# Kernel tuning notes

Measured on AMD Instinct MI355X. Metric: run time of the kernel, lower is better.

Reference implementation:

```python
import jax, jax.numpy as jnp
import numpy as np

N_USER = 100_000
N_WALLET = 100_000
E = 1_600_000
HID, OUT = 128, 64
H, C = 4, 32  # GAT heads, per-head channels (HID // 4)
U_IN, W_IN = 16, 4
EPS = 1e-5


def _sage(x_src, x_dst, ei, w_l, b_l, w_r):
    """PyG SAGEConv (mean aggr): lin_l(mean_j x_j) + lin_r(x_i)."""
    src, dst = ei[0], ei[1]
    n = x_dst.shape[0]
    s = jax.ops.segment_sum(x_src[src], dst, num_segments=n)
    deg = jax.ops.segment_sum(jnp.ones((src.shape[0],), x_src.dtype), dst, num_segments=n)
    agg = s / jnp.maximum(deg, 1.0)[:, None]
    return agg @ w_l + b_l + x_dst @ w_r


def _bn(x, g, b):
    """BatchNorm over node dim (training-mode batch stats)."""
    m = x.mean(0)
    v = x.var(0)
    return (x - m) * jax.lax.rsqrt(v + EPS) * g + b


def _segment_softmax(logits, seg, n):
    m = jax.ops.segment_max(logits, seg, num_segments=n)
    e = jnp.exp(logits - m[seg])
    s = jax.ops.segment_sum(e, seg, num_segments=n)
    return e / (s[seg] + 1e-16)


def _gat(x, ei, w, a_src, a_dst, bias):
    """PyG GATConv with self-loops, heads concatenated. Dropout off (eval)."""
    n = x.shape[0]
    loop = jnp.arange(n, dtype=ei.dtype)
    src = jnp.concatenate([ei[0], loop])
    dst = jnp.concatenate([ei[1], loop])
    xp = (x @ w).reshape(n, H, C)                      # [n,H,C]
    al_s = (xp * a_src).sum(-1)                        # [n,H]
    al_d = (xp * a_dst).sum(-1)                        # [n,H]
    logits = jax.nn.leaky_relu(al_s[src] + al_d[dst], 0.2)  # [E+n,H]
    alpha = _segment_softmax(logits, dst, n)
    out = jax.ops.segment_sum(xp[src] * alpha[:, :, None], dst, num_segments=n)
    return out.reshape(n, H * C) + bias


def setup_inputs() -> dict:
    key = jax.random.key(0)
    ks = jax.random.split(key, 24)
    rn = lambda k, s, sc=0.05: jax.random.normal(k, s, jnp.float32) * sc
    ei = lambda k, n: jax.random.randint(k, (2, E), 0, n, jnp.int32)
    return {
        "x_user": rn(ks[0], (N_USER, U_IN), 1.0),
        "x_wallet": rn(ks[1], (N_WALLET, W_IN), 1.0),
        "w_u2w_l": rn(ks[2], (U_IN, HID)), "b_u2w": jnp.zeros((HID,), jnp.float32), "w_u2w_r": rn(ks[3], (W_IN, HID)),
        "w_w2u_l": rn(ks[4], (W_IN, HID)), "b_w2u": jnp.zeros((HID,), jnp.float32), "w_w2u_r": rn(ks[5], (U_IN, HID)),
        "w_u2u_l": rn(ks[6], (U_IN, HID)), "b_u2u": jnp.zeros((HID,), jnp.float32), "w_u2u_r": rn(ks[7], (U_IN, HID)),
        "bn_u_g": jnp.ones((HID,), jnp.float32), "bn_u_b": jnp.zeros((HID,), jnp.float32),
        "bn_w_g": jnp.ones((HID,), jnp.float32), "bn_w_b": jnp.zeros((HID,), jnp.float32),
        "gat_w": rn(ks[8], (HID, H * C)), "gat_as": rn(ks[9], (H, C)), "gat_ad": rn(ks[10], (H, C)),
        "gat_b": jnp.zeros((HID,), jnp.float32),
        "bn2_g": jnp.ones((HID,), jnp.float32), "bn2_b": jnp.zeros((HID,), jnp.float32),
        "proj_w": rn(ks[11], (HID, OUT)), "proj_b": jnp.zeros((OUT,), jnp.float32),
        "ei_uw": ei(ks[12], N_USER),   # src user -> dst wallet (both 100k)
        "ei_wu": ei(ks[13], N_WALLET),  # src wallet -> dst user
        "ei_uu": ei(ks[14], N_USER),
    }


def reference(x_user, x_wallet, w_u2w_l, b_u2w, w_u2w_r, w_w2u_l, b_w2u, w_w2u_r,
              w_u2u_l, b_u2u, w_u2u_r, bn_u_g, bn_u_b, bn_w_g, bn_w_b,
              gat_w, gat_as, gat_ad, gat_b, bn2_g, bn2_b, proj_w, proj_b,
              ei_uw, ei_wu, ei_uu):
    h_w_from_u = jax.nn.relu(_sage(x_user, x_wallet, ei_uw, w_u2w_l, b_u2w, w_u2w_r))
    h_u_from_w = jax.nn.relu(_sage(x_wallet, x_user, ei_wu, w_w2u_l, b_w2u, w_w2u_r))
    h_u_from_u = jax.nn.relu(_sage(x_user, x_user, ei_uu, w_u2u_l, b_u2u, w_u2u_r))
    h_user = _bn(h_u_from_w + h_u_from_u, bn_u_g, bn_u_b)
    _ = _bn(h_w_from_u, bn_w_g, bn_w_b)  # h_wallet: computed in torch module but unused in output
    h_user = jax.nn.relu(_gat(h_user, ei_uu, gat_w, gat_as, gat_ad, gat_b))
    h_user = _bn(h_user, bn2_g, bn2_b)
    return jax.nn.relu(h_user @ proj_w + proj_b)  # dropout = identity (eval)
```

## Files before the change

kernel.cpp:

```cpp
#include <hip/hip_runtime.h>
#include <hip/hip_bf16.h>
#include <cstdint>
#include <cstddef>

#define NN   100000
#define NE   1600000
#define CAP  48

#define NBKT 784
#define BSH  7
#define FB   8
#define BCAP 2432
#define ACHUNK 2048
#define NABLK 784

#define NTILES 1563
#define CH_BN 500
#define LOG2E 1.44269504088896f

typedef __attribute__((ext_vector_type(8))) short short8;
typedef __attribute__((ext_vector_type(4))) float floatx4;

__device__ inline short f2bs(float x) {
    __hip_bfloat16 h = __float2bfloat16(x);
    return *reinterpret_cast<short*>(&h);
}
__device__ inline int pack2(float a, float b) {
    return ((int)(unsigned short)f2bs(b) << 16) | (unsigned short)f2bs(a);
}
__device__ inline float bflo(unsigned p) { return __uint_as_float(p << 16); }
__device__ inline float bfhi(unsigned p) { return __uint_as_float(p & 0xFFFF0000u); }

#define OFF_PRE   ((size_t)0)
#define OFF_BKTU  ((size_t)0)
#define OFF_BKTW  ((size_t)1906688)
#define OFF_XP    ((size_t)12800000)
#define OFF_AGGU  ((size_t)12800000)
#define OFF_AGGW  ((size_t)14400000)
#define OFF_COLU  ((size_t)19200000)
#define OFF_CNTU  ((size_t)25600000)
#define OFF_BCUR  ((size_t)25800000)
#define OFF_S1    ((size_t)25801600)
#define OFF_Q1    ((size_t)25801728)
#define OFF_S2    ((size_t)25801856)
#define OFF_Q2    ((size_t)25801984)
#define OFF_ALS   ((size_t)25802112)
#define OFF_ALD   ((size_t)26202112)
#define ZBASE     OFF_BCUR
#define ZFLOATS   ((size_t)2112)

__global__ void __launch_bounds__(256) bin_edges(
    const int* __restrict__ ei_u, const int* __restrict__ ei_w,
    int* __restrict__ bcur_u, int* __restrict__ bkt_u,
    int* __restrict__ bcur_w, int* __restrict__ bkt_w) {
    const int* ei = blockIdx.y ? ei_w : ei_u;
    int* bcur = blockIdx.y ? bcur_w : bcur_u;
    int* bkt  = blockIdx.y ? bkt_w  : bkt_u;
    __shared__ int lcnt[NBKT];
    __shared__ int lbuf[NBKT * FB];
    for (int i = threadIdx.x; i < NBKT; i += 256) lcnt[i] = 0;
    __syncthreads();
    int base = blockIdx.x * ACHUNK;
    #pragma unroll
    for (int k = 0; k < ACHUNK / 256; k++) {
        int e = base + k * 256 + threadIdx.x;
        if (e < NE) {
            int src = ei[e], dst = ei[NE + e];
            int b = dst >> BSH;
            int pk = ((dst & ((1 << BSH) - 1)) << 17) | src;
            int pos = atomicAdd(&lcnt[b], 1);
            if (pos < FB) lbuf[b * FB + pos] = pk;
            else {
                int g = atomicAdd(&bcur[b], 1);
                if (g < BCAP) bkt[(size_t)b * BCAP + g] = pk;
            }
        }
    }
    __syncthreads();
    int wid = threadIdx.x >> 6, lane = threadIdx.x & 63;
    const int BPW = NBKT / 4;
    int b0w = wid * BPW;
    for (int r = 0; r < BPW; r += 64) {
        int rb = r + lane;
        if (rb < BPW) {
            int b = b0w + rb;
            int c = lcnt[b];
            int nn2 = c < FB ? c : FB;
            if (nn2 > 0) {
                int g0 = atomicAdd(&bcur[b], nn2);
                for (int i2 = 0; i2 < nn2; i2++) {
                    int g = g0 + i2;
                    if (g < BCAP) bkt[(size_t)b * BCAP + g] = lbuf[b * FB + i2];
                }
            }
        }
    }
}

__global__ void __launch_bounds__(256) csr_agg(
    const int* __restrict__ bcur_u, const int* __restrict__ bkt_u,
    int* __restrict__ cnt_g, int* __restrict__ col_g,
    const float* __restrict__ xu, float* __restrict__ aggu,
    const int* __restrict__ bcur_w, const int* __restrict__ bkt_w,
    const float* __restrict__ xw, float* __restrict__ aggw) {
    int type = blockIdx.y;
    const int* bcur = type ? bcur_w : bcur_u;
    const int* bkt  = type ? bkt_w  : bkt_u;
    int B = blockIdx.x;
    int node_base = B << BSH;
    if (node_base >= NN) return;
    __shared__ int cnt[128];
    __shared__ int col[128 * CAP];
    if (threadIdx.x < 128) cnt[threadIdx.x] = 0;
    __syncthreads();
    int n = bcur[B]; if (n > BCAP) n = BCAP;
    const int* bp = bkt + (size_t)B * BCAP;
    for (int i = threadIdx.x; i < n; i += 256) {
        int p = bp[i];
        int d = p >> 17;
        int pos = atomicAdd(&cnt[d], 1);
        if (pos < CAP) col[d * CAP + pos] = p & 0x1FFFF;
    }
    __syncthreads();
    int nn_here = NN - node_base; if (nn_here > 128) nn_here = 128;
    int wv = threadIdx.x >> 6, lane = threadIdx.x & 63;

    if (type == 0) {
        if (threadIdx.x < nn_here) cnt_g[node_base + threadIdx.x] = cnt[threadIdx.x];
        int total4 = nn_here * CAP / 4;
        const int4* cs = (const int4*)col;
        int4* cg = (int4*)(col_g + (size_t)node_base * CAP);
        for (int i = threadIdx.x; i < total4; i += 256) cg[i] = cs[i];
        int j = lane >> 4, k = lane & 15;
        for (int nl = wv * 32; nl < wv * 32 + 32 && nl < nn_here; nl++) {
            int deg = cnt[nl];
            int nu = deg < CAP ? deg : CAP;
            float v0 = 0.f, v1 = 0.f, v2 = 0.f, v3 = 0.f;
            int iters = (nu + 15) >> 4;
            for (int it = 0; it < iters; it++) {
                int bb = j + (it << 4);
                int s0 = (bb < nu)      ? col[nl * CAP + bb]      : 0;
                int s1 = (bb + 4 < nu)  ? col[nl * CAP + bb + 4]  : 0;
                int s2 = (bb + 8 < nu)  ? col[nl * CAP + bb + 8]  : 0;
                int s3 = (bb + 12 < nu) ? col[nl * CAP + bb + 12] : 0;
                float x0 = xu[(size_t)s0 * 16 + k];
                float x1 = xu[(size_t)s1 * 16 + k];
                float x2 = xu[(size_t)s2 * 16 + k];
                float x3 = xu[(size_t)s3 * 16 + k];
                if (bb < nu)      v0 += x0;
                if (bb + 4 < nu)  v1 += x1;
                if (bb + 8 < nu)  v2 += x2;
                if (bb + 12 < nu) v3 += x3;
            }
            float v = (v0 + v1) + (v2 + v3);
            v += __shfl_xor(v, 16, 64);
            v += __shfl_xor(v, 32, 64);
            if (lane < 16)
                aggu[(size_t)(node_base + nl) * 16 + lane] = v / fmaxf((float)deg, 1.f);
        }
    } else {
        int j = lane >> 2, k = lane & 3;
        for (int nl = wv * 32; nl < wv * 32 + 32 && nl < nn_here; nl++) {
            int deg = cnt[nl];
            int nw = deg < CAP ? deg : CAP;
            float v = 0.f;
            int iters = (nw + 15) >> 4;
            for (int it = 0; it < iters; it++) {
                int bb = j + (it << 4);
                int s = (bb < nw) ? col[nl * CAP + bb] : 0;
                float x = xw[(size_t)s * 4 + k];
                if (bb < nw) v += x;
            }
            v += __shfl_xor(v, 4, 64);
            v += __shfl_xor(v, 8, 64);
            v += __shfl_xor(v, 16, 64);
            v += __shfl_xor(v, 32, 64);
            if (lane < 4)
                aggw[(size_t)(node_base + nl) * 4 + lane] = v / fmaxf((float)deg, 1.f);
        }
    }
}

__global__ void __launch_bounds__(256, 2) sage_gemm(
    const float* __restrict__ aggu, const float* __restrict__ aggw,
    const float* __restrict__ xu,
    const float* __restrict__ wl_w2u, const float* __restrict__ b_w2u, const float* __restrict__ wr_w2u,
    const float* __restrict__ wl_u2u, const float* __restrict__ b_u2u, const float* __restrict__ wr_u2u,
    __hip_bfloat16* __restrict__ pre) {
    __shared__ short lw[16 * 64 * 8];
    __shared__ short la[64 * 136];
    int tid = threadIdx.x;
    for (int idx = tid; idx < 8192; idx += 256) {
        int mat = idx >> 12;
        int k = (idx >> 7) & 31, n = idx & 127;
        float w;
        if (mat == 0)
            w = (k < 4) ? wl_w2u[k * 128 + n] : (k < 20 ? wr_w2u[(k - 4) * 128 + n] : 0.f);
        else
            w = (k < 16) ? wl_u2u[k * 128 + n] : wr_u2u[(k - 16) * 128 + n];
        int t = n >> 4, l15 = n & 15, q = (k >> 3) & 3, j = k & 7;
        lw[((mat * 8 + t) * 64 + q * 16 + l15) * 8 + j] = f2bs(w);
    }
    __syncthreads();
    int wv = tid >> 6, lane = tid & 63;
    int quad = lane >> 4, l15 = lane & 15;
    short8 w1[8], w2[8];
    #pragma unroll
    for (int t = 0; t < 8; t++) {
        w1[t] = *(const short8*)&lw[(t * 64 + lane) * 8];
        w2[t] = *(const short8*)&lw[((8 + t) * 64 + lane) * 8];
    }
    float bw[8], bu[8];
    #pragma unroll
    for (int t = 0; t < 8; t++) {
        bw[t] = b_w2u[t * 16 + l15];
        bu[t] = b_u2u[t * 16 + l15];
    }
    for (int tile = blockIdx.x; tile < NTILES; tile += gridDim.x) {
        int nbase = tile * 64;
        __syncthreads();
        {
            int node = tid >> 2, p = tid & 3;
            int gn = nbase + node;
            float4 v = make_float4(0.f, 0.f, 0.f, 0.f);
            if (gn < NN) v = *(const float4*)&xu[(size_t)gn * 16 + 4 * p];
            int2 pk; pk.x = pack2(v.x, v.y); pk.y = pack2(v.z, v.w);
            *(int2*)&la[node * 136 + 4 + 4 * p] = pk;
            *(int2*)&la[node * 136 + 48 + 4 * p] = pk;
        }
        {
            int node = tid >> 2, p = tid & 3;
            int gn = nbase + node;
            float4 v = make_float4(0.f, 0.f, 0.f, 0.f);
            if (gn < NN) v = *(const float4*)&aggu[(size_t)gn * 16 + 4 * p];
            int2 pk; pk.x = pack2(v.x, v.y); pk.y = pack2(v.z, v.w);
            *(int2*)&la[node * 136 + 32 + 4 * p] = pk;
        }
        if (tid < 64) {
            int node = tid, gn = nbase + node;
            float4 v = make_float4(0.f, 0.f, 0.f, 0.f);
            if (gn < NN) v = *(const float4*)&aggw[(size_t)gn * 4];
            int2 pk; pk.x = pack2(v.x, v.y); pk.y = pack2(v.z, v.w);
            *(int2*)&la[node * 136 + 0] = pk;
            int2 z; z.x = 0; z.y = 0;
            *(int2*)&la[node * 136 + 20] = z;
            *(int2*)&la[node * 136 + 24] = z;
            *(int2*)&la[node * 136 + 28] = z;
        }
        __syncthreads();
        short8 af1 = *(const short8*)&la[(wv * 16 + l15) * 136 + quad * 8];
        short8 af2 = *(const short8*)&la[(wv * 16 + l15) * 136 + 32 + quad * 8];
        floatx4 acc1[8], acc2[8];
        #pragma unroll
        for (int t = 0; t < 8; t++) {
            acc1[t] = (floatx4){0.f, 0.f, 0.f, 0.f};
            acc2[t] = (floatx4){0.f, 0.f, 0.f, 0.f};
        }
        #pragma unroll
        for (int t = 0; t < 8; t++) {
            acc1[t] = __builtin_amdgcn_mfma_f32_16x16x32_bf16(af1, w1[t], acc1[t], 0, 0, 0);
            acc2[t] = __builtin_amdgcn_mfma_f32_16x16x32_bf16(af2, w2[t], acc2[t], 0, 0, 0);
        }
        __syncthreads();
        #pragma unroll
        for (int t = 0; t < 8; t++)
            #pragma unroll
            for (int r = 0; r < 4; r++) {
                float v1 = fmaxf(acc1[t][r] + bw[t], 0.f);
                float v2 = fmaxf(acc2[t][r] + bu[t], 0.f);
                la[(wv * 16 + quad * 4 + r) * 136 + t * 16 + l15] = f2bs(v1 + v2);
            }
        __syncthreads();
        #pragma unroll
        for (int c = 0; c < 4; c++) {
            int idx = c * 256 + tid;
            int node = idx >> 4, f8 = (idx & 15) * 8;
            int gn = nbase + node;
            if (gn < NN)
                *(int4*)(pre + (size_t)gn * 128 + f8) = *(const int4*)&la[node * 136 + f8];
        }
    }
}

__global__ void __launch_bounds__(256) bn_stats_pre2(const unsigned* __restrict__ x2,
                                                     float* __restrict__ sum, float* __restrict__ sq) {
    int f2 = threadIdx.x & 63, half = threadIdx.x >> 6;
    int n0 = blockIdx.x * CH_BN;
    float s0 = 0.f, q0 = 0.f, s1 = 0.f, q1 = 0.f;
    for (int i = n0 + half; i < n0 + CH_BN; i += 4) {
        unsigned p = x2[(size_t)i * 64 + f2];
        float v0 = bflo(p), v1 = bfhi(p);
        s0 += v0; q0 += v0 * v0; s1 += v1; q1 += v1 * v1;
    }
    __shared__ float a0[256], c0[256], a1[256], c1[256];
    a0[threadIdx.x] = s0; c0[threadIdx.x] = q0;
    a1[threadIdx.x] = s1; c1[threadIdx.x] = q1;
    __syncthreads();
    if (half == 0) {
        for (int h = 1; h < 4; h++) {
            s0 += a0[h * 64 + f2]; q0 += c0[h * 64 + f2];
            s1 += a1[h * 64 + f2]; q1 += c1[h * 64 + f2];
        }
        atomicAdd(&sum[2 * f2], s0);     atomicAdd(&sq[2 * f2], q0);
        atomicAdd(&sum[2 * f2 + 1], s1); atomicAdd(&sq[2 * f2 + 1], q1);
    }
}

__global__ void __launch_bounds__(256) bn_stats_act2(const unsigned* __restrict__ x2,
                                                     const float* __restrict__ gb,
                                                     float* __restrict__ sum, float* __restrict__ sq) {
    int f2 = threadIdx.x & 63, half = threadIdx.x >> 6;
    int n0 = blockIdx.x * CH_BN;
    float gb0 = gb[2 * f2], gb1 = gb[2 * f2 + 1];
    float s0 = 0.f, q0 = 0.f, s1 = 0.f, q1 = 0.f;
    for (int i = n0 + half; i < n0 + CH_BN; i += 4) {
        unsigned p = x2[(size_t)i * 64 + f2];
        float v0 = fmaxf(bflo(p) + gb0, 0.f), v1 = fmaxf(bfhi(p) + gb1, 0.f);
        s0 += v0; q0 += v0 * v0; s1 += v1; q1 += v1 * v1;
    }
    __shared__ float a0[256], c0[256], a1[256], c1[256];
    a0[threadIdx.x] = s0; c0[threadIdx.x] = q0;
    a1[threadIdx.x] = s1; c1[threadIdx.x] = q1;
    __syncthreads();
    if (half == 0) {
        for (int h = 1; h < 4; h++) {
            s0 += a0[h * 64 + f2]; q0 += c0[h * 64 + f2];
            s1 += a1[h * 64 + f2]; q1 += c1[h * 64 + f2];
        }
        atomicAdd(&sum[2 * f2], s0);     atomicAdd(&sq[2 * f2], q0);
        atomicAdd(&sum[2 * f2 + 1], s1); atomicAdd(&sq[2 * f2 + 1], q1);
    }
}

__global__ void __launch_bounds__(256, 2) gemm_al(
    const unsigned* __restrict__ pre2, const float* __restrict__ s1, const float* __restrict__ q1,
    const float* __restrict__ bng, const float* __restrict__ bnb,
    const float* __restrict__ gw, const float* __restrict__ gas, const float* __restrict__ gad,
    __hip_bfloat16* __restrict__ xp, float* __restrict__ al_s, float* __restrict__ al_d) {
    __shared__ short lw[32 * 64 * 8];
    __shared__ short la[64 * 136];
    __shared__ float lsc[128], lsh[128];
    int tid = threadIdx.x;
    if (tid < 128) {
        float m = s1[tid] * (1.0f / NN);
        float v = q1[tid] * (1.0f / NN) - m * m;
        float sc = bng[tid] * rsqrtf(v + 1e-5f);
        lsc[tid] = sc; lsh[tid] = bnb[tid] - m * sc;
    }
    for (int idx = tid; idx < 16384; idx += 256) {
        int k = idx >> 7, n = idx & 127;
        int t = n >> 4, l15 = n & 15, s = k >> 5, q = (k >> 3) & 3, j = k & 7;
        lw[(((t * 4 + s) * 64) + q * 16 + l15) * 8 + j] = f2bs(gw[idx]);
    }
    __syncthreads();
    int wv = tid >> 6, lane = tid & 63;
    int quad = lane >> 4, l15 = lane & 15;
    short8 wfrag[8][4];
    #pragma unroll
    for (int t = 0; t < 8; t++)
        #pragma unroll
        for (int s = 0; s < 4; s++)
            wfrag[t][s] = *(const short8*)&lw[((t * 4 + s) * 64 + lane) * 8];
    float asv[8], adv[8];
    #pragma unroll
    for (int t = 0; t < 8; t++) {
        asv[t] = gas[t * 16 + l15] * LOG2E;
        adv[t] = gad[t * 16 + l15] * LOG2E;
    }
    for (int tile = blockIdx.x; tile < NTILES; tile += gridDim.x) {
        int nbase = tile * 64;
        __syncthreads();
        #pragma unroll
        for (int c = 0; c < 8; c++) {
            int idx = c * 256 + tid;
            int node = idx >> 5, g = idx & 31;
            uint2 pp = make_uint2(0u, 0u);
            int gn = nbase + node;
            if (gn < NN) pp = *(const uint2*)&pre2[(size_t)gn * 64 + 2 * g];
            int f = 4 * g;
            float v0 = bflo(pp.x), v1 = bfhi(pp.x), v2 = bflo(pp.y), v3 = bfhi(pp.y);
            int2 pk;
            pk.x = pack2(v0 * lsc[f] + lsh[f],         v1 * lsc[f + 1] + lsh[f + 1]);
            pk.y = pack2(v2 * lsc[f + 2] + lsh[f + 2], v3 * lsc[f + 3] + lsh[f + 3]);
            *(int2*)&la[node * 136 + f] = pk;
        }
        __syncthreads();
        short8 af[4];
        #pragma unroll
        for (int s = 0; s < 4; s++)
            af[s] = *(const short8*)&la[(wv * 16 + l15) * 136 + s * 32 + quad * 8];
        floatx4 acc[8];
        #pragma unroll
        for (int t = 0; t < 8; t++) acc[t] = (floatx4){0.f, 0.f, 0.f, 0.f};
        #pragma unroll
        for (int s = 0; s < 4; s++)
            #pragma unroll
            for (int t = 0; t < 8; t++)
                acc[t] = __builtin_amdgcn_mfma_f32_16x16x32_bf16(af[s], wfrag[t][s], acc[t], 0, 0, 0);
        #pragma unroll
        for (int r = 0; r < 4; r++) {
            int node = nbase + wv * 16 + quad * 4 + r;
            #pragma unroll
            for (int h = 0; h < 4; h++) {
                float vs = acc[2 * h][r] * asv[2 * h] + acc[2 * h + 1][r] * asv[2 * h + 1];
                float vd = acc[2 * h][r] * adv[2 * h] + acc[2 * h + 1][r] * adv[2 * h + 1];
                #pragma unroll
                for (int m = 8; m >= 1; m >>= 1) {
                    vs += __shfl_xor(vs, m, 64);
                    vd += __shfl_xor(vd, m, 64);
                }
                if (l15 == 0 && node < NN) {
                    al_s[(size_t)node * 4 + h] = vs;
                    al_d[(size_t)node * 4 + h] = vd;
                }
            }
        }
        __syncthreads();
        #pragma unroll
        for (int t = 0; t < 8; t++)
            #pragma unroll
            for (int r = 0; r < 4; r++)
                la[(wv * 16 + quad * 4 + r) * 136 + t * 16 + l15] = f2bs(acc[t][r]);
        __syncthreads();
        #pragma unroll
        for (int c = 0; c < 4; c++) {
            int idx = c * 256 + tid;
            int node = idx >> 4, f8 = (idx & 15) * 8;
            int gn = nbase + node;
            if (gn < NN)
                *(int4*)(xp + (size_t)gn * 128 + f8) = *(const int4*)&la[node * 136 + f8];
        }
    }
}

__global__ void __launch_bounds__(256, 2) gemm_proj(
    const unsigned* __restrict__ gat2, const float* __restrict__ gb,
    const float* __restrict__ s2, const float* __restrict__ q2,
    const float* __restrict__ bng, const float* __restrict__ bnb,
    const float* __restrict__ pw, const float* __restrict__ pb,
    float* __restrict__ out) {
    __shared__ short lw[16 * 64 * 8];
    __shared__ short la[64 * 136];
    __shared__ float lsc[128], lsh[128], lgb[128];
    int tid = threadIdx.x;
    if (tid < 128) {
        float m = s2[tid] * (1.0f / NN);
        float v = q2[tid] * (1.0f / NN) - m * m;
        float sc = bng[tid] * rsqrtf(v + 1e-5f);
        lsc[tid] = sc; lsh[tid] = bnb[tid] - m * sc;
        lgb[tid] = gb[tid];
    }
    for (int idx = tid; idx < 8192; idx += 256) {
        int k = idx >> 6, n = idx & 63;
        int t = n >> 4, l15 = n & 15, s = k >> 5, q = (k >> 3) & 3, j = k & 7;
        lw[(((t * 4 + s) * 64) + q * 16 + l15) * 8 + j] = f2bs(pw[idx]);
    }
    __syncthreads();
    int wv = tid >> 6, lane = tid & 63;
    int quad = lane >> 4, l15 = lane & 15;
    short8 wfrag[4][4];
    #pragma unroll
    for (int t = 0; t < 4; t++)
        #pragma unroll
        for (int s = 0; s < 4; s++)
            wfrag[t][s] = *(const short8*)&lw[((t * 4 + s) * 64 + lane) * 8];
    float pbv[4];
    #pragma unroll
    for (int t = 0; t < 4; t++) pbv[t] = pb[t * 16 + l15];
    for (int tile = blockIdx.x; tile < NTILES; tile += gridDim.x) {
        int nbase = tile * 64;
        __syncthreads();
        #pragma unroll
        for (int c = 0; c < 8; c++) {
            int idx = c * 256 + tid;
            int node = idx >> 5, g = idx & 31;
            uint2 pp = make_uint2(0u, 0u);
            int gn = nbase + node;
            if (gn < NN) pp = *(const uint2*)&gat2[(size_t)gn * 64 + 2 * g];
            int f = 4 * g;
            float h0 = fmaxf(bflo(pp.x) + lgb[f],     0.f) * lsc[f]     + lsh[f];
            float h1 = fmaxf(bfhi(pp.x) + lgb[f + 1], 0.f) * lsc[f + 1] + lsh[f + 1];
            float h2 = fmaxf(bflo(pp.y) + lgb[f + 2], 0.f) * lsc[f + 2] + lsh[f + 2];
            float h3 = fmaxf(bfhi(pp.y) + lgb[f + 3], 0.f) * lsc[f + 3] + lsh[f + 3];
            int2 pk; pk.x = pack2(h0, h1); pk.y = pack2(h2, h3);
            *(int2*)&la[node * 136 + f] = pk;
        }
        __syncthreads();
        short8 af[4];
        #pragma unroll
        for (int s = 0; s < 4; s++)
            af[s] = *(const short8*)&la[(wv * 16 + l15) * 136 + s * 32 + quad * 8];
        floatx4 acc[4];
        #pragma unroll
        for (int t = 0; t < 4; t++) acc[t] = (floatx4){0.f, 0.f, 0.f, 0.f};
        #pragma unroll
        for (int s = 0; s < 4; s++)
            #pragma unroll
            for (int t = 0; t < 4; t++)
                acc[t] = __builtin_amdgcn_mfma_f32_16x16x32_bf16(af[s], wfrag[t][s], acc[t], 0, 0, 0);
        #pragma unroll
        for (int r = 0; r < 4; r++) {
            int gn = nbase + wv * 16 + quad * 4 + r;
            if (gn < NN) {
                #pragma unroll
                for (int t = 0; t < 4; t++)
                    out[(size_t)gn * 64 + t * 16 + l15] = fmaxf(acc[t][r] + pbv[t], 0.f);
            }
        }
    }
}

__global__ void __launch_bounds__(256) gat_gather(
    const int* __restrict__ cnt_u, const int* __restrict__ col_u,
    const float* __restrict__ al_s, const float* __restrict__ al_d,
    const unsigned* __restrict__ xp2, unsigned* __restrict__ gout2) {
    int i = (blockIdx.x * 256 + threadIdx.x) >> 6;
    int lane = threadIdx.x & 63;
    int g = lane >> 4, q = lane & 15;
    int h = q >> 2;
    float ad = al_d[(size_t)i * 4 + h];
    int deg = cnt_u[i];
    int n = deg < CAP ? deg : CAP;
    int mycol = (lane < n) ? col_u[(size_t)i * CAP + lane] : 0;
    float a0 = 0.f, a1 = 0.f, a2 = 0.f, a3 = 0.f;
    float a4 = 0.f, a5 = 0.f, a6 = 0.f, a7 = 0.f, den = 0.f;
    if (g == 0) {
        float l = al_s[(size_t)i * 4 + h] + ad;
        float e = exp2f(fmaxf(l, 0.2f * l));
        uint4 p = *(const uint4*)&xp2[(size_t)i * 64 + 4 * q];
        a0 = e * bflo(p.x); a1 = e * bfhi(p.x);
        a2 = e * bflo(p.y); a3 = e * bfhi(p.y);
        a4 = e * bflo(p.z); a5 = e * bfhi(p.z);
        a6 = e * bflo(p.w); a7 = e * bfhi(p.w);
        den = e;
    }
    for (int b = 0; b < n; b += 16) {
        int s[4]; float A[4]; uint4 p[4];
        #pragma unroll
        for (int u = 0; u < 4; u++)
            s[u] = __shfl(mycol, b + 4 * u + g, 64);
        #pragma unroll
        for (int u = 0; u < 4; u++)
            A[u] = al_s[(size_t)s[u] * 4 + h];
        #pragma unroll
        for (int u = 0; u < 4; u++)
            p[u] = *(const uint4*)&xp2[(size_t)s[u] * 64 + 4 * q];
        #pragma unroll
        for (int u = 0; u < 4; u++) {
            float l = A[u] + ad;
            float e = (b + 4 * u + g < n) ? exp2f(fmaxf(l, 0.2f * l)) : 0.f;
            a0 += e * bflo(p[u].x); a1 += e * bfhi(p[u].x);
            a2 += e * bflo(p[u].y); a3 += e * bfhi(p[u].y);
            a4 += e * bflo(p[u].z); a5 += e * bfhi(p[u].z);
            a6 += e * bflo(p[u].w); a7 += e * bfhi(p[u].w);
            den += e;
        }
    }
    a0 += __shfl_xor(a0, 16, 64); a0 += __shfl_xor(a0, 32, 64);
    a1 += __shfl_xor(a1, 16, 64); a1 += __shfl_xor(a1, 32, 64);
    a2 += __shfl_xor(a2, 16, 64); a2 += __shfl_xor(a2, 32, 64);
    a3 += __shfl_xor(a3, 16, 64); a3 += __shfl_xor(a3, 32, 64);
    a4 += __shfl_xor(a4, 16, 64); a4 += __shfl_xor(a4, 32, 64);
    a5 += __shfl_xor(a5, 16, 64); a5 += __shfl_xor(a5, 32, 64);
    a6 += __shfl_xor(a6, 16, 64); a6 += __shfl_xor(a6, 32, 64);
    a7 += __shfl_xor(a7, 16, 64); a7 += __shfl_xor(a7, 32, 64);
    den += __shfl_xor(den, 16, 64); den += __shfl_xor(den, 32, 64);
    if (g == 0) {
        float r = 1.0f / (den + 1e-16f);
        uint4 o;
        o.x = (unsigned)pack2(a0 * r, a1 * r);
        o.y = (unsigned)pack2(a2 * r, a3 * r);
        o.z = (unsigned)pack2(a4 * r, a5 * r);
        o.w = (unsigned)pack2(a6 * r, a7 * r);
        *(uint4*)&gout2[(size_t)i * 64 + 4 * q] = o;
    }
}

extern "C" void kernel_launch(void* const* d_in, const int* in_sizes, int n_in,
                              void* d_out, int out_size, void* d_ws, size_t ws_size,
                              hipStream_t stream) {
    const float* x_user   = (const float*)d_in[0];
    const float* x_wallet = (const float*)d_in[1];
    const float* w_w2u_l  = (const float*)d_in[5];
    const float* b_w2u    = (const float*)d_in[6];
    const float* w_w2u_r  = (const float*)d_in[7];
    const float* w_u2u_l  = (const float*)d_in[8];
    const float* b_u2u    = (const float*)d_in[9];
    const float* w_u2u_r  = (const float*)d_in[10];
    const float* bn_u_g   = (const float*)d_in[11];
    const float* bn_u_b   = (const float*)d_in[12];
    const float* gat_w    = (const float*)d_in[15];
    const float* gat_as   = (const float*)d_in[16];
    const float* gat_ad   = (const float*)d_in[17];
    const float* gat_b    = (const float*)d_in[18];
    const float* bn2_g    = (const float*)d_in[19];
    const float* bn2_b    = (const float*)d_in[20];
    const float* proj_w   = (const float*)d_in[21];
    const float* proj_b   = (const float*)d_in[22];
    const int* ei_wu      = (const int*)d_in[24];
    const int* ei_uu      = (const int*)d_in[25];
    float* out = (float*)d_out;
    float* ws  = (float*)d_ws;

    unsigned* pre2 = (unsigned*)(ws + OFF_PRE);
    __hip_bfloat16* pre = (__hip_bfloat16*)(ws + OFF_PRE);
    int*   bkt_u  = (int*)(ws + OFF_BKTU);
    int*   bkt_w  = (int*)(ws + OFF_BKTW);
    __hip_bfloat16* xp = (__hip_bfloat16*)(ws + OFF_XP);
    unsigned* xp2 = (unsigned*)(ws + OFF_XP);
    float* aggu = ws + OFF_AGGU;
    float* aggw = ws + OFF_AGGW;
    int*   col_u  = (int*)(ws + OFF_COLU);
    int*   cnt_u  = (int*)(ws + OFF_CNTU);
    int*   bcur_u = (int*)(ws + OFF_BCUR);
    int*   bcur_w = (int*)(ws + OFF_BCUR) + 800;
    float* al_s = ws + OFF_ALS, *al_d = ws + OFF_ALD;
    float* s1 = ws + OFF_S1, *q1 = ws + OFF_Q1;
    float* s2 = ws + OFF_S2, *q2 = ws + OFF_Q2;

    hipMemsetAsync(ws + ZBASE, 0, ZFLOATS * sizeof(float), stream);

    bin_edges<<<dim3(NABLK, 2), 256, 0, stream>>>(ei_uu, ei_wu, bcur_u, bkt_u, bcur_w, bkt_w);

    csr_agg<<<dim3(NBKT, 2), 256, 0, stream>>>(
        bcur_u, bkt_u, cnt_u, col_u, x_user, aggu,
        bcur_w, bkt_w, x_wallet, aggw);

    sage_gemm<<<512, 256, 0, stream>>>(
        aggu, aggw, x_user, w_w2u_l, b_w2u, w_w2u_r, w_u2u_l, b_u2u, w_u2u_r, pre);

    bn_stats_pre2<<<NN / CH_BN, 256, 0, stream>>>(pre2, s1, q1);

    gemm_al<<<512, 256, 0, stream>>>(pre2, s1, q1, bn_u_g, bn_u_b,
                                     gat_w, gat_as, gat_ad, xp, al_s, al_d);

    unsigned* gat2 = pre2;
    gat_gather<<<NN / 4, 256, 0, stream>>>(cnt_u, col_u, al_s, al_d, xp2, gat2);

    bn_stats_act2<<<NN / CH_BN, 256, 0, stream>>>(gat2, gat_b, s2, q2);

    gemm_proj<<<512, 256, 0, stream>>>(gat2, gat_b, s2, q2, bn2_g, bn2_b,
                                       proj_w, proj_b, out);
}
```

Baseline: 475.0 us.

## Restructure GAT gather into block-tiled kernel with precomputed attention weights and fused BN stats

```diff
diff --git a/kernel.cpp b/kernel.cpp
--- a/kernel.cpp
+++ b/kernel.cpp
@@ -1,5 +1,6 @@
 #include <hip/hip_runtime.h>
 #include <hip/hip_bf16.h>
+#include <hip/hip_fp16.h>
 #include <cstdint>
 #include <cstddef>
 
@@ -17,6 +18,9 @@
 #define NTILES 1563
 #define CH_BN 500
 #define LOG2E 1.44269504088896f
+
+#define GSLOT 49
+#define NGBLK 782
 
 typedef __attribute__((ext_vector_type(8))) short short8;
 typedef __attribute__((ext_vector_type(4))) float floatx4;
@@ -306,32 +310,6 @@
     }
 }
 
-__global__ void __launch_bounds__(256) bn_stats_act2(const unsigned* __restrict__ x2,
-                                                     const float* __restrict__ gb,
-                                                     float* __restrict__ sum, float* __restrict__ sq) {
-    int f2 = threadIdx.x & 63, half = threadIdx.x >> 6;
-    int n0 = blockIdx.x * CH_BN;
-    float gb0 = gb[2 * f2], gb1 = gb[2 * f2 + 1];
-    float s0 = 0.f, q0 = 0.f, s1 = 0.f, q1 = 0.f;
-    for (int i = n0 + half; i < n0 + CH_BN; i += 4) {
-        unsigned p = x2[(size_t)i * 64 + f2];
-        float v0 = fmaxf(bflo(p) + gb0, 0.f), v1 = fmaxf(bfhi(p) + gb1, 0.f);
-        s0 += v0; q0 += v0 * v0; s1 += v1; q1 += v1 * v1;
-    }
-    __shared__ float a0[256], c0[256], a1[256], c1[256];
-    a0[threadIdx.x] = s0; c0[threadIdx.x] = q0;
-    a1[threadIdx.x] = s1; c1[threadIdx.x] = q1;
-    __syncthreads();
-    if (half == 0) {
-        for (int h = 1; h < 4; h++) {
-            s0 += a0[h * 64 + f2]; q0 += c0[h * 64 + f2];
-            s1 += a1[h * 64 + f2]; q1 += c1[h * 64 + f2];
-        }
-        atomicAdd(&sum[2 * f2], s0);     atomicAdd(&sq[2 * f2], q0);
-        atomicAdd(&sum[2 * f2 + 1], s1); atomicAdd(&sq[2 * f2 + 1], q1);
-    }
-}
-
 __global__ void __launch_bounds__(256, 2) gemm_al(
     const unsigned* __restrict__ pre2, const float* __restrict__ s1, const float* __restrict__ q1,
     const float* __restrict__ bng, const float* __restrict__ bnb,
@@ -510,69 +488,116 @@
     }
 }
 
-__global__ void __launch_bounds__(256) gat_gather(
+__global__ void __launch_bounds__(256, 2) gat_gather(
     const int* __restrict__ cnt_u, const int* __restrict__ col_u,
     const float* __restrict__ al_s, const float* __restrict__ al_d,
-    const unsigned* __restrict__ xp2, unsigned* __restrict__ gout2) {
-    int i = (blockIdx.x * 256 + threadIdx.x) >> 6;
-    int lane = threadIdx.x & 63;
+    const unsigned* __restrict__ xp2, unsigned* __restrict__ gout2,
+    const float* __restrict__ gb, float* __restrict__ s2g, float* __restrict__ q2g) {
+    __shared__ int    lcol[128 * GSLOT];
+    __shared__ ushort le[128 * GSLOT * 4];
+    __shared__ float  lad[128 * 4];
+    __shared__ int    lm[128];
+    __shared__ float  lss[128], lqq[128];
+    int tid = threadIdx.x;
+    int base = blockIdx.x * 128;
+    int nmax = NN - base; if (nmax > 128) nmax = 128; if (nmax < 0) nmax = 0;
+
+    if (tid < 128) {
+        int gi = base + tid;
+        int d = 0;
+        if (tid < nmax) {
+            d = cnt_u[gi]; if (d > CAP) d = CAP;
+            *(float4*)&lad[tid * 4] = *(const float4*)&al_d[(size_t)gi * 4];
+        }
+        lm[tid] = (tid < nmax) ? d + 1 : 0;
+        lss[tid] = 0.f; lqq[tid] = 0.f;
+    }
+    for (int idx = tid; idx < nmax * CAP; idx += 256) {
+        int nl = idx / CAP, sl = idx - nl * CAP;
+        lcol[nl * GSLOT + sl] = col_u[(size_t)base * CAP + idx];
+    }
+    __syncthreads();
+    if (tid < nmax) lcol[tid * GSLOT + (lm[tid] - 1)] = base + tid;
+    __syncthreads();
+
+    for (int idx = tid; idx < 128 * GSLOT; idx += 256) {
+        int nl = idx / GSLOT, sl = idx - nl * GSLOT;
+        if (sl < lm[nl]) {
+            int s = lcol[idx];
+            float4 as4 = *(const float4*)&al_s[(unsigned)s * 4];
+            float l0 = as4.x + lad[nl * 4 + 0];
+            float l1 = as4.y + lad[nl * 4 + 1];
+            float l2 = as4.z + lad[nl * 4 + 2];
+            float l3 = as4.w + lad[nl * 4 + 3];
+            float e0 = exp2f(fmaxf(l0, 0.2f * l0));
+            float e1 = exp2f(fmaxf(l1, 0.2f * l1));
+            float e2 = exp2f(fmaxf(l2, 0.2f * l2));
+            float e3 = exp2f(fmaxf(l3, 0.2f * l3));
+            unsigned w0 = ((unsigned)__half_as_ushort(__float2half(e1)) << 16)
+                        |  (unsigned)__half_as_ushort(__float2half(e0));
+            unsigned w1 = ((unsigned)__half_as_ushort(__float2half(e3)) << 16)
+                        |  (unsigned)__half_as_ushort(__float2half(e2));
+            uint2 pk; pk.x = w0; pk.y = w1;
+            *(uint2*)&le[idx * 4] = pk;
+        }
+    }
+    __syncthreads();
+
+    int wv = tid >> 6, lane = tid & 63;
     int g = lane >> 4, q = lane & 15;
-    int h = q >> 2;
-    float ad = al_d[(size_t)i * 4 + h];
-    int deg = cnt_u[i];
-    int n = deg < CAP ? deg : CAP;
-    int mycol = (lane < n) ? col_u[(size_t)i * CAP + lane] : 0;
-    float a0 = 0.f, a1 = 0.f, a2 = 0.f, a3 = 0.f;
-    float a4 = 0.f, a5 = 0.f, a6 = 0.f, a7 = 0.f, den = 0.f;
-    if (g == 0) {
-        float l = al_s[(size_t)i * 4 + h] + ad;
-        float e = exp2f(fmaxf(l, 0.2f * l));
-        uint4 p = *(const uint4*)&xp2[(size_t)i * 64 + 4 * q];
-        a0 = e * bflo(p.x); a1 = e * bfhi(p.x);
-        a2 = e * bflo(p.y); a3 = e * bfhi(p.y);
-        a4 = e * bflo(p.z); a5 = e * bfhi(p.z);
-        a6 = e * bflo(p.w); a7 = e * bfhi(p.w);
-        den = e;
-    }
-    for (int b = 0; b < n; b += 16) {
-        int s[4]; float A[4]; uint4 p[4];
-        #pragma unroll
-        for (int u = 0; u < 4; u++)
-            s[u] = __shfl(mycol, b + 4 * u + g, 64);
-        #pragma unroll
-        for (int u = 0; u < 4; u++)
-            A[u] = al_s[(size_t)s[u] * 4 + h];
-        #pragma unroll
-        for (int u = 0; u < 4; u++)
-            p[u] = *(const uint4*)&xp2[(size_t)s[u] * 64 + 4 * q];
-        #pragma unroll
-        for (int u = 0; u < 4; u++) {
-            float l = A[u] + ad;
-            float e = (b + 4 * u + g < n) ? exp2f(fmaxf(l, 0.2f * l)) : 0.f;
-            a0 += e * bflo(p[u].x); a1 += e * bfhi(p[u].x);
-            a2 += e * bflo(p[u].y); a3 += e * bfhi(p[u].y);
-            a4 += e * bflo(p[u].z); a5 += e * bfhi(p[u].z);
-            a6 += e * bflo(p[u].w); a7 += e * bfhi(p[u].w);
-            den += e;
-        }
-    }
-    a0 += __shfl_xor(a0, 16, 64); a0 += __shfl_xor(a0, 32, 64);
-    a1 += __shfl_xor(a1, 16, 64); a1 += __shfl_xor(a1, 32, 64);
-    a2 += __shfl_xor(a2, 16, 64); a2 += __shfl_xor(a2, 32, 64);
-    a3 += __shfl_xor(a3, 16, 64); a3 += __shfl_xor(a3, 32, 64);
-    a4 += __shfl_xor(a4, 16, 64); a4 += __shfl_xor(a4, 32, 64);
-    a5 += __shfl_xor(a5, 16, 64); a5 += __shfl_xor(a5, 32, 64);
-    a6 += __shfl_xor(a6, 16, 64); a6 += __shfl_xor(a6, 32, 64);
-    a7 += __shfl_xor(a7, 16, 64); a7 += __shfl_xor(a7, 32, 64);
-    den += __shfl_xor(den, 16, 64); den += __shfl_xor(den, 32, 64);
-    if (g == 0) {
-        float r = 1.0f / (den + 1e-16f);
-        uint4 o;
-        o.x = (unsigned)pack2(a0 * r, a1 * r);
-        o.y = (unsigned)pack2(a2 * r, a3 * r);
-        o.z = (unsigned)pack2(a4 * r, a5 * r);
-        o.w = (unsigned)pack2(a6 * r, a7 * r);
-        *(uint4*)&gout2[(size_t)i * 64 + 4 * q] = o;
+    #pragma unroll
+    for (int h = 0; h < 4; h++) {
+        float gb0 = gb[h * 32 + 2 * q], gb1 = gb[h * 32 + 2 * q + 1];
+        float sE = 0.f, qE = 0.f, sO = 0.f, qO = 0.f;
+        for (int nl = wv * 32; nl < wv * 32 + 32; nl++) {
+            if (nl >= nmax) break;
+            int m = lm[nl];
+            float a0 = 0.f, a1 = 0.f, den = 0.f;
+            for (int b = 0; b < m; b += 16) {
+                int s_[4]; float e_[4]; unsigned p_[4];
+                #pragma unroll
+                for (int u = 0; u < 4; u++) {
+                    int sl = b + 4 * u + g;
+                    bool v = sl < m;
+                    int slc = v ? sl : 0;
+                    s_[u] = lcol[nl * GSLOT + slc];
+                    ushort eu = le[(nl * GSLOT + slc) * 4 + h];
+                    float e = __half2float(__ushort_as_half(eu));
+                    e_[u] = v ? e : 0.f;
+                }
+                #pragma unroll
+                for (int u = 0; u < 4; u++)
+                    p_[u] = xp2[(unsigned)s_[u] * 64 + h * 16 + q];
+                #pragma unroll
+                for (int u = 0; u < 4; u++) {
+                    a0 += e_[u] * bflo(p_[u]);
+                    a1 += e_[u] * bfhi(p_[u]);
+                    den += e_[u];
+                }
+            }
+            a0 += __shfl_xor(a0, 16, 64); a0 += __shfl_xor(a0, 32, 64);
+            a1 += __shfl_xor(a1, 16, 64); a1 += __shfl_xor(a1, 32, 64);
+            den += __shfl_xor(den, 16, 64); den += __shfl_xor(den, 32, 64);
+            if (g == 0) {
+                float r = 1.0f / (den + 1e-16f);
+                unsigned pk = (unsigned)pack2(a0 * r, a1 * r);
+                gout2[(size_t)(base + nl) * 64 + h * 16 + q] = pk;
+                float v0 = fmaxf(bflo(pk) + gb0, 0.f);
+                float v1 = fmaxf(bfhi(pk) + gb1, 0.f);
+                sE += v0; qE += v0 * v0; sO += v1; qO += v1 * v1;
+            }
+        }
+        if (g == 0) {
+            atomicAdd(&lss[h * 32 + 2 * q],     sE);
+            atomicAdd(&lqq[h * 32 + 2 * q],     qE);
+            atomicAdd(&lss[h * 32 + 2 * q + 1], sO);
+            atomicAdd(&lqq[h * 32 + 2 * q + 1], qO);
+        }
+    }
+    __syncthreads();
+    if (tid < 128) {
+        atomicAdd(&s2g[tid], lss[tid]);
+        atomicAdd(&q2g[tid], lqq[tid]);
     }
 }
 
@@ -635,9 +660,8 @@
                                      gat_w, gat_as, gat_ad, xp, al_s, al_d);
 
     unsigned* gat2 = pre2;
-    gat_gather<<<NN / 4, 256, 0, stream>>>(cnt_u, col_u, al_s, al_d, xp2, gat2);
-
-    bn_stats_act2<<<NN / CH_BN, 256, 0, stream>>>(gat2, gat_b, s2, q2);
+    gat_gather<<<NGBLK, 256, 0, stream>>>(cnt_u, col_u, al_s, al_d, xp2, gat2,
+                                          gat_b, s2, q2);
 
     gemm_proj<<<512, 256, 0, stream>>>(gat2, gat_b, s2, q2, bn2_g, bn2_b,
                                        proj_w, proj_b, out);
```

Result: slower. 650.0 us (+36.9%).
